# Kernel optimization log

Hardware: AMD Instinct MI355X
Metric: run time of the kernel (lower is better)

Reference implementation:

```python
import jax, jax.numpy as jnp
import numpy as np

EMBED = 256
HEADS = 8
HEAD_DIM = EMBED // HEADS  # 32, even for RoPE
INIT_VAL = 1.0
HEADS_RANGE = 3.0


def rotate_every_two(x):
    # (x1, x2) -> (-x2, x1) on interleaved pairs of last dim
    x1 = x[..., ::2]
    x2 = x[..., 1::2]
    return jnp.stack([-x2, x1], axis=-1).reshape(x.shape)


def theta_shift(x, sin, cos):
    # x: [B, heads, H, W, D]; sin/cos: [H, W, D] broadcast over B, heads
    return x * cos + rotate_every_two(x) * sin


def rel_pos_2d(H, W):
    # RetNetRelPos2d: RoPE angles + per-head exponential decay mask
    angle = 1.0 / (10000.0 ** jnp.linspace(0.0, 1.0, HEAD_DIM // 2))
    angle = jnp.repeat(angle, 2)  # [D]
    idx = jnp.arange(H * W, dtype=jnp.float32)
    sin = jnp.sin(idx[:, None] * angle[None, :]).reshape(H, W, HEAD_DIM)
    cos = jnp.cos(idx[:, None] * angle[None, :]).reshape(H, W, HEAD_DIM)
    h_idx = jnp.arange(HEADS, dtype=jnp.float32)
    decay = jnp.log(1.0 - 2.0 ** (-INIT_VAL - HEADS_RANGE * h_idx / HEADS))  # [heads]
    gh, gw = jnp.meshgrid(jnp.arange(H), jnp.arange(W), indexing='ij')
    grid = jnp.stack([gh, gw], axis=-1).reshape(H * W, 2)  # [N,2]
    dist = jnp.abs(grid[:, None, :] - grid[None, :, :]).sum(-1)  # [N,N] L1 distance
    mask = dist[None, :, :].astype(jnp.float32) * decay[:, None, None]  # [heads,N,N]
    return sin, cos, mask


def setup_inputs() -> dict:
    key = jax.random.key(0)
    ks = jax.random.split(key, 8)
    B, H, W, C = 2, 48, 48, EMBED
    s = 0.02
    return {
        'x': jax.random.normal(ks[0], (B, H, W, C), jnp.float32),
        'Wq': jax.random.normal(ks[1], (C, C), jnp.float32) * s,
        'bq': jnp.zeros((C,), jnp.float32),
        'Wk': jax.random.normal(ks[2], (C, C), jnp.float32) * s,
        'bk': jnp.zeros((C,), jnp.float32),
        'Wv': jax.random.normal(ks[3], (C, C), jnp.float32) * s,
        'bv': jnp.zeros((C,), jnp.float32),
        'lepe_w': jax.random.normal(ks[4], (C, 1, 5, 5), jnp.float32) * s,  # depthwise 5x5
        'lepe_b': jnp.zeros((C,), jnp.float32),
        'Wo': jax.random.normal(ks[5], (C, C), jnp.float32) * s,
        'bo': jnp.zeros((C,), jnp.float32),
    }


def reference(x, Wq, bq, Wk, bk, Wv, bv, lepe_w, lepe_b, Wo, bo):
    B, H, W, C = x.shape
    N = H * W
    sin, cos, mask = rel_pos_2d(H, W)
    scaling = HEAD_DIM ** -0.5

    q = x @ Wq + bq
    k = (x @ Wk + bk) * scaling
    v = x @ Wv + bv

    # lepe: depthwise 5x5 conv on v (BHWC)
    lepe = jax.lax.conv_general_dilated(
        v.transpose(0, 3, 1, 2), lepe_w, (1, 1), 'SAME',
        feature_group_count=C, dimension_numbers=('NCHW', 'OIHW', 'NCHW'))
    lepe = lepe.transpose(0, 2, 3, 1) + lepe_b  # [B,H,W,C]

    def split_heads(t):
        return t.reshape(B, H, W, HEADS, HEAD_DIM).transpose(0, 3, 1, 2, 4)

    qr = theta_shift(split_heads(q), sin, cos).reshape(B, HEADS, N, HEAD_DIM)
    kr = theta_shift(split_heads(k), sin, cos).reshape(B, HEADS, N, HEAD_DIM)
    vv = split_heads(v).reshape(B, HEADS, N, HEAD_DIM)

    attn = jnp.einsum('bhnd,bhmd->bhnm', qr, kr) + mask[None]  # [B,heads,N,N]
    attn = jax.nn.softmax(attn, axis=-1)
    out = jnp.einsum('bhnm,bhmd->bhnd', attn, vv)
    out = out.transpose(0, 2, 1, 3).reshape(B, H, W, C)
    out = out + lepe
    return out @ Wo + bo
```

## Files before the change

### kernel.cpp

```cpp
#include <hip/hip_runtime.h>
#include <hip/hip_bf16.h>
#include <math.h>

#define NN 2304
#define ROWSZ 4608
#define SZ (ROWSZ*256)

typedef __attribute__((ext_vector_type(8))) short short8;
typedef __attribute__((ext_vector_type(4))) float f32x4;

__device__ __forceinline__ float bf2f(unsigned short u) {
    return __uint_as_float(((unsigned int)u) << 16);
}
__device__ __forceinline__ unsigned short f2bf(float f) {
    unsigned int u = __float_as_uint(f);
    u += 0x7FFFu + ((u >> 16) & 1u);
    return (unsigned short)(u >> 16);
}
__device__ __forceinline__ unsigned int pack_bf2(float a, float b) {
    return (unsigned int)f2bf(a) | ((unsigned int)f2bf(b) << 16);
}

__device__ __forceinline__ float ub2f(unsigned int v, int r) {
#if defined(__has_builtin)
#if __has_builtin(__builtin_amdgcn_cvt_f32_ubyte0)
    switch (r) {
        case 0: return __builtin_amdgcn_cvt_f32_ubyte0(v);
        case 1: return __builtin_amdgcn_cvt_f32_ubyte1(v);
        case 2: return __builtin_amdgcn_cvt_f32_ubyte2(v);
        default: return __builtin_amdgcn_cvt_f32_ubyte3(v);
    }
#else
    return (float)((v >> (8*r)) & 0xFFu);
#endif
#else
    return (float)((v >> (8*r)) & 0xFFu);
#endif
}

template<int F32>
__device__ __forceinline__ float ldin(const void* p, int i) {
    if constexpr (F32) return ((const float*)p)[i];
    else return bf2f(((const unsigned short*)p)[i]);
}

__global__ void detect_kernel(const unsigned int* __restrict__ x, int* __restrict__ flag) {
    int t = threadIdx.x;
    int cnt = 0;
    for (int i = t; i < 256; i += 64) {
        unsigned int e = (x[i] >> 7) & 0xFFu;
        cnt += (e < 87u || e > 167u) ? 1 : 0;
    }
    #pragma unroll
    for (int o = 32; o; o >>= 1) cnt += __shfl_down(cnt, o);
    if (t == 0) *flag = (cnt >= 32) ? 1 : 0;
}

__global__ __launch_bounds__(256) void dist_kernel(unsigned char* __restrict__ D) {
    const int nq = blockIdx.x;
    const int yq = (nq*21846) >> 20, xq = nq - yq*48;
    unsigned int* drow = reinterpret_cast<unsigned int*>(D + (size_t)nq*NN);
    for (int idx = threadIdx.x; idx < 576; idx += 256) {
        const int kp0 = idx*4;
        unsigned int wv = 0;
        #pragma unroll
        for (int r = 0; r < 4; ++r) {
            int kp = kp0 + r;
            int yk = (kp*21846) >> 20;
            int xk = kp - yk*48;
            unsigned int dist = __usad((unsigned)yq, (unsigned)yk,
                                __usad((unsigned)xq, (unsigned)xk, 0u));
            wv |= dist << (8*r);
        }
        drow[idx] = wv;
    }
}

template<int F32>
__device__ __forceinline__ void qkv_body(
    const void* __restrict__ x,
    const void* __restrict__ Wq, const void* __restrict__ bq,
    const void* __restrict__ Wk, const void* __restrict__ bk,
    const void* __restrict__ Wv, const void* __restrict__ bv,
    unsigned short* __restrict__ q, unsigned short* __restrict__ k,
    unsigned short* __restrict__ v, unsigned short* __restrict__ vT,
    float* __restrict__ xs)
{
    const int t = threadIdx.x;
    const int by = blockIdx.y;
    const int row0 = blockIdx.x * 16;
    #pragma unroll
    for (int pass = 0; pass < 2; ++pass) {
        int e = pass*2048 + t*8;
        if constexpr (F32) {
            const float* xp = (const float*)x + row0*256 + e;
            float4 a0 = *reinterpret_cast<const float4*>(xp);
            float4 a1 = *reinterpret_cast<const float4*>(xp + 4);
            *reinterpret_cast<float4*>(&xs[e])   = a0;
            *reinterpret_cast<float4*>(&xs[e+4]) = a1;
        } else {
            const unsigned short* xp = (const unsigned short*)x + row0*256 + e;
            uint4 raw = *reinterpret_cast<const uint4*>(xp);
            const unsigned short* us = reinterpret_cast<const unsigned short*>(&raw);
            #pragma unroll
            for (int j = 0; j < 8; ++j) xs[e + j] = bf2f(us[j]);
        }
    }
    __syncthreads();
    const void* Wsel = (by == 0) ? Wq : (by == 1) ? Wk : Wv;
    const void* bsel = (by == 0) ? bq : (by == 1) ? bk : bv;
    float a[16];
    const float bv0 = ldin<F32>(bsel, t);
    #pragma unroll
    for (int r = 0; r < 16; ++r) a[r] = bv0;
    for (int i0 = 0; i0 < 256; i0 += 4) {
        float w0 = ldin<F32>(Wsel, (i0+0)*256 + t);
        float w1 = ldin<F32>(Wsel, (i0+1)*256 + t);
        float w2 = ldin<F32>(Wsel, (i0+2)*256 + t);
        float w3 = ldin<F32>(Wsel, (i0+3)*256 + t);
        #pragma unroll
        for (int r = 0; r < 16; ++r) {
            float4 xv = *reinterpret_cast<const float4*>(&xs[r*256 + i0]);
            a[r] = fmaf(xv.w,w3, fmaf(xv.z,w2, fmaf(xv.y,w1, fmaf(xv.x,w0, a[r]))));
        }
    }
    if (by == 2) {
        const int b = (row0 >= NN) ? 1 : 0;
        const int n0 = row0 - b*NN;
        const int h = t >> 5, d = t & 31;
        unsigned int vp[8];
        #pragma unroll
        for (int r = 0; r < 16; ++r) v[(row0 + r)*256 + t] = f2bf(a[r]);
        #pragma unroll
        for (int r = 0; r < 8; ++r) vp[r] = pack_bf2(a[2*r], a[2*r+1]);
        unsigned short* vt = vT + ((size_t)(b*8 + h)*32 + d)*NN + n0;
        *reinterpret_cast<uint4*>(vt)     = make_uint4(vp[0], vp[1], vp[2], vp[3]);
        *reinterpret_cast<uint4*>(vt + 8) = make_uint4(vp[4], vp[5], vp[6], vp[7]);
    } else {
        const float scaling = 0.17677669529663687f;
        const float log2e   = 1.4426950408889634f;
        const int j = (t & 31) >> 1;
        const float ang = exp2f((float)j * (-0.8858474919699633f));
        const bool odd = t & 1;
        unsigned short* dst = (by == 0) ? q : k;
        const float mul = (by == 0) ? 1.0f : scaling * log2e;
        #pragma unroll
        for (int r = 0; r < 16; ++r) {
            int bn = row0 + r;
            int n = bn >= NN ? bn - NN : bn;
            float sv, cv;
            sincosf((float)n * ang, &sv, &cv);
            float ap = __shfl_xor(a[r], 1);
            float val = odd ? fmaf(a[r], cv, ap*sv) : fmaf(a[r], cv, -ap*sv);
            dst[bn*256 + t] = f2bf(val * mul);
        }
    }
}

__global__ __launch_bounds__(256) void qkv_kernel(
    const void* __restrict__ x,
    const void* __restrict__ Wq, const void* __restrict__ bq,
    const void* __restrict__ Wk, const void* __restrict__ bk,
    const void* __restrict__ Wv, const void* __restrict__ bv,
    const int* __restrict__ flag,
    unsigned short* __restrict__ q, unsigned short* __restrict__ k,
    unsigned short* __restrict__ v, unsigned short* __restrict__ vT)
{
    __shared__ float xs[16*256];
    if (*flag) qkv_body<1>(x, Wq, bq, Wk, bk, Wv, bv, q, k, v, vT, xs);
    else       qkv_body<0>(x, Wq, bq, Wk, bk, Wv, bv, q, k, v, vT, xs);
}

template<int F32>
__device__ __forceinline__ void lepe_body(const unsigned short* __restrict__ v,
    const void* __restrict__ w, const void* __restrict__ wb,
    unsigned short* __restrict__ lepe)
{
    int c = threadIdx.x;
    int pos = blockIdx.x;
    int b  = pos >= NN ? 1 : 0;
    int yx = pos - b*NN;
    int y  = (yx*21846) >> 20;
    int xx = yx - y*48;
    float acc = ldin<F32>(wb, c);
    #pragma unroll
    for (int ky = 0; ky < 5; ++ky) {
        int yy = y + ky - 2;
        if ((unsigned)yy >= 48u) continue;
        #pragma unroll
        for (int kx = 0; kx < 5; ++kx) {
            int xc = xx + kx - 2;
            if ((unsigned)xc >= 48u) continue;
            acc = fmaf(bf2f(v[((b*NN + yy*48 + xc)<<8) + c]), ldin<F32>(w, c*25 + ky*5 + kx), acc);
        }
    }
    lepe[(pos<<8) + c] = f2bf(acc);
}

__global__ __launch_bounds__(256) void lepe_kernel(const unsigned short* __restrict__ v,
    const void* __restrict__ w, const void* __restrict__ wb,
    const int* __restrict__ flag, unsigned short* __restrict__ lepe)
{
    if (*flag) lepe_body<1>(v, w, wb, lepe);
    else       lepe_body<0>(v, w, wb, lepe);
}

template<int DIRECT>
__global__ __launch_bounds__(256) void attn_kernel(
    const unsigned short* __restrict__ q, const unsigned short* __restrict__ k,
    const unsigned short* __restrict__ vT, const unsigned char* __restrict__ D,
    unsigned short* __restrict__ o, float* __restrict__ pacc, float* __restrict__ pl)
{
    __shared__ char smem[27648];
    const int t = threadIdx.x;
    const int w = t >> 6, lane = t & 63;
    const int q16 = lane & 15, quad = lane >> 4;
    char* PsB = smem + 19456 + w*2048;
    const int bh = blockIdx.y, b = bh >> 3, h = bh & 7;
    const int q0 = blockIdx.x*64 + w*16;
    const int nq = q0 + q16;
    const float decay2 = log2f(1.0f - exp2f(-1.0f - 0.375f*(float)h));
    short8 qfrag = *reinterpret_cast<const short8*>(q + ((size_t)(b*NN + nq))*256 + h*32 + quad*8);
    f32x4 acc0 = {0.f,0.f,0.f,0.f}, acc1 = {0.f,0.f,0.f,0.f};
    const f32x4 zero = {0.f,0.f,0.f,0.f};
    float lacc = 0.0f;
    const unsigned short* kbase = k + (size_t)(b*NN)*256 + h*32;
    const unsigned short* vtb = vT + (size_t)bh*32*NN;
    const unsigned char* Dbase = D + (size_t)nq*NN + quad*4;
    const int skr = t >> 2, skp = t & 3;
    const int svd = t >> 3, svp = t & 7;
    const int psW = q16*16 + (quad & 1)*8;
    const int qsh = quad >> 1;
    const int nchunk = 36 / gridDim.z;
    const int kt0 = blockIdx.z * nchunk;

    {
        uint4 kraw = *reinterpret_cast<const uint4*>(kbase + (kt0*64 + skr)*256 + skp*8);
        uint4 vraw = *reinterpret_cast<const uint4*>(vtb + svd*NN + kt0*64 + svp*8);
        *reinterpret_cast<uint4*>(smem + skr*80 + skp*16) = kraw;
        *reinterpret_cast<uint4*>(smem + 5120 + svd*144 + svp*16) = vraw;
    }
    __syncthreads();

    int cur = 0;
    for (int kc = 0; kc < nchunk; ++kc) {
        const int kt = kt0 + kc;
        const int ktn = (kc + 1 < nchunk) ? kt + 1 : kt;
        uint4 nk = *reinterpret_cast<const uint4*>(kbase + (ktn*64 + skr)*256 + skp*8);
        uint4 nv = *reinterpret_cast<const uint4*>(vtb + svd*NN + ktn*64 + svp*8);
        unsigned int dw[4];
        #pragma unroll
        for (int tt = 0; tt < 4; ++tt)
            dw[tt] = *reinterpret_cast<const unsigned int*>(Dbase + kt*64 + tt*16);
        char* KsB = smem + cur*9728;
        char* VtB = KsB + 5120;
        f32x4 st[4];
        #pragma unroll
        for (int tt = 0; tt < 4; ++tt) {
            short8 kf = *reinterpret_cast<const short8*>(KsB + (tt*16 + q16)*80 + quad*16);
            st[tt] = __builtin_amdgcn_mfma_f32_16x16x32_bf16(kf, qfrag, zero, 0, 0, 0);
        }
        unsigned int pk[8];
        float lsum = 0.0f;
        #pragma unroll
        for (int tt = 0; tt < 4; ++tt) {
            float p[4];
            #pragma unroll
            for (int r = 0; r < 4; ++r) {
                p[r] = exp2f(fmaf(decay2, ub2f(dw[tt], r), st[tt][r]));
                lsum += p[r];
            }
            pk[tt*2]   = __builtin_amdgcn_perm(__float_as_uint(p[1]), __float_as_uint(p[0]), 0x07060302);
            pk[tt*2+1] = __builtin_amdgcn_perm(__float_as_uint(p[3]), __float_as_uint(p[2]), 0x07060302);
        }
        lacc += lsum;
        #pragma unroll
        for (int tt = 0; tt < 4; ++tt) {
            uint2 pp; pp.x = pk[tt*2]; pp.y = pk[tt*2+1];
            *reinterpret_cast<uint2*>(PsB + (tt >> 1)*1024 + (((tt*2) + qsh) & 3)*256 + psW) = pp;
        }
        #pragma unroll
        for (int kh = 0; kh < 2; ++kh) {
            short8 pf = *reinterpret_cast<const short8*>(PsB + kh*1024 + lane*16);
            short8 v0 = *reinterpret_cast<const short8*>(VtB + q16*144 + kh*64 + quad*16);
            short8 v1 = *reinterpret_cast<const short8*>(VtB + (16 + q16)*144 + kh*64 + quad*16);
            acc0 = __builtin_amdgcn_mfma_f32_16x16x32_bf16(v0, pf, acc0, 0, 0, 0);
            acc1 = __builtin_amdgcn_mfma_f32_16x16x32_bf16(v1, pf, acc1, 0, 0, 0);
        }
        char* KsN = smem + (cur^1)*9728;
        *reinterpret_cast<uint4*>(KsN + skr*80 + skp*16) = nk;
        *reinterpret_cast<uint4*>(KsN + 5120 + svd*144 + svp*16) = nv;
        __syncthreads();
        cur ^= 1;
    }
    lacc += __shfl_xor(lacc, 16);
    lacc += __shfl_xor(lacc, 32);
    if constexpr (DIRECT) {
        float invl = 1.0f / lacc;
        unsigned short* orow = o + ((size_t)(b*NN + nq))*256 + h*32;
        uint2 w0, w1;
        w0.x = pack_bf2(acc0[0]*invl, acc0[1]*invl);
        w0.y = pack_bf2(acc0[2]*invl, acc0[3]*invl);
        w1.x = pack_bf2(acc1[0]*invl, acc1[1]*invl);
        w1.y = pack_bf2(acc1[2]*invl, acc1[3]*invl);
        *reinterpret_cast<uint2*>(orow + quad*4)      = w0;
        *reinterpret_cast<uint2*>(orow + 16 + quad*4) = w1;
    } else {
        float* pb = pacc + ((size_t)(blockIdx.z*16 + bh)*NN + nq)*32;
        *reinterpret_cast<f32x4*>(pb + quad*4)      = acc0;
        *reinterpret_cast<f32x4*>(pb + 16 + quad*4) = acc1;
        if (quad == 0) pl[((size_t)blockIdx.z*16 + bh)*NN + nq] = lacc;
    }
}

template<int F32>
__device__ __forceinline__ void out_body(
    const unsigned short* __restrict__ o,
    const float* __restrict__ pacc, const float* __restrict__ pl,
    const unsigned short* __restrict__ lp,
    const void* __restrict__ Wo, const void* __restrict__ bo,
    void* __restrict__ out, float* __restrict__ as, int nsplit)
{
    const int t = threadIdx.x;
    const int row0 = blockIdx.x * 8;
    {
        const int e = t*8;
        const int r = t >> 5;
        const int nqr = row0 + r;
        const int ch = e & 255;
        uint4 ub = *reinterpret_cast<const uint4*>(lp + nqr*256 + ch);
        const unsigned short* bu = reinterpret_cast<const unsigned short*>(&ub);
        if (nsplit == 0) {
            uint4 ua = *reinterpret_cast<const uint4*>(o + nqr*256 + ch);
            const unsigned short* au = reinterpret_cast<const unsigned short*>(&ua);
            #pragma unroll
            for (int jj = 0; jj < 8; ++jj) as[e+jj] = bf2f(au[jj]) + bf2f(bu[jj]);
        } else {
            const int b = nqr >= NN ? 1 : 0;
            const int nq = nqr - b*NN;
            const int h = ch >> 5, d = ch & 31;
            const int bh = b*8 + h;
            float s[8] = {0.f,0.f,0.f,0.f,0.f,0.f,0.f,0.f};
            float lsum = 0.0f;
            for (int p = 0; p < nsplit; ++p) {
                const float* pb = pacc + ((size_t)(p*16 + bh)*NN + nq)*32 + d;
                f32x4 v0 = *reinterpret_cast<const f32x4*>(pb);
                f32x4 v1 = *reinterpret_cast<const f32x4*>(pb + 4);
                #pragma unroll
                for (int jj = 0; jj < 4; ++jj) { s[jj] += v0[jj]; s[4+jj] += v1[jj]; }
                lsum += pl[((size_t)p*16 + bh)*NN + nq];
            }
            float invl = 1.0f / lsum;
            #pragma unroll
            for (int jj = 0; jj < 8; ++jj) as[e+jj] = fmaf(s[jj], invl, bf2f(bu[jj]));
        }
    }
    __syncthreads();
    float a[8];
    const float bv = ldin<F32>(bo, t);
    #pragma unroll
    for (int r = 0; r < 8; ++r) a[r] = bv;
    for (int i0 = 0; i0 < 256; i0 += 4) {
        float w0 = ldin<F32>(Wo, (i0+0)*256 + t);
        float w1 = ldin<F32>(Wo, (i0+1)*256 + t);
        float w2 = ldin<F32>(Wo, (i0+2)*256 + t);
        float w3 = ldin<F32>(Wo, (i0+3)*256 + t);
        #pragma unroll
        for (int r = 0; r < 8; ++r) {
            float4 xv = *reinterpret_cast<const float4*>(&as[r*256 + i0]);
            a[r] = fmaf(xv.w,w3, fmaf(xv.z,w2, fmaf(xv.y,w1, fmaf(xv.x,w0, a[r]))));
        }
    }
    #pragma unroll
    for (int r = 0; r < 8; ++r) {
        int idx = (row0+r)*256 + t;
        if constexpr (F32) ((float*)out)[idx] = a[r];
        else ((unsigned short*)out)[idx] = f2bf(a[r]);
    }
}

__global__ __launch_bounds__(256) void out_kernel(
    const unsigned short* __restrict__ o,
    const float* __restrict__ pacc, const float* __restrict__ pl,
    const unsigned short* __restrict__ lp,
    const void* __restrict__ Wo, const void* __restrict__ bo,
    const int* __restrict__ flag, void* __restrict__ out, int nsplit)
{
    __shared__ float as[8*256];
    if (*flag) out_body<1>(o, pacc, pl, lp, Wo, bo, out, as, nsplit);
    else       out_body<0>(o, pacc, pl, lp, Wo, bo, out, as, nsplit);
}

extern "C" void kernel_launch(void* const* d_in, const int* in_sizes, int n_in,
                              void* d_out, int out_size, void* d_ws, size_t ws_size,
                              hipStream_t stream)
{
    const void* x  = d_in[0];
    const void* Wq = d_in[1];
    const void* bq = d_in[2];
    const void* Wk = d_in[3];
    const void* bk = d_in[4];
    const void* Wv = d_in[5];
    const void* bv = d_in[6];
    const void* lw = d_in[7];
    const void* lb = d_in[8];
    const void* Wo = d_in[9];
    const void* bo = d_in[10];

    int* flag = (int*)d_ws;
    unsigned short* qb   = (unsigned short*)((char*)d_ws + 256);
    unsigned short* kbuf = qb   + (size_t)SZ;
    unsigned short* vbuf = kbuf + (size_t)SZ;
    unsigned short* obuf = vbuf + (size_t)SZ;
    unsigned short* lbuf = obuf + (size_t)SZ;
    unsigned short* vtb  = lbuf + (size_t)SZ;
    unsigned char*  Dtab = (unsigned char*)(vtb + (size_t)SZ);

    const size_t base = 256 + 6*(size_t)SZ*2 + (size_t)NN*NN;
    const size_t per_split = (size_t)16*NN*32*4 + (size_t)16*NN*4;
    int nsplit = 0;
    if      (ws_size >= base + 4*per_split) nsplit = 4;
    else if (ws_size >= base + 2*per_split) nsplit = 2;
    else if (ws_size >= base + 1*per_split) nsplit = 1;
    float* pacc = (float*)((char*)d_ws + base);
    float* pl   = pacc + (size_t)(nsplit ? nsplit : 1)*16*NN*32;

    detect_kernel<<<1, 64, 0, stream>>>((const unsigned int*)x, flag);
    dist_kernel<<<NN, 256, 0, stream>>>(Dtab);
    qkv_kernel<<<dim3(288,3), 256, 0, stream>>>(x, Wq, bq, Wk, bk, Wv, bv, flag, qb, kbuf, vbuf, vtb);
    lepe_kernel<<<4608, 256, 0, stream>>>(vbuf, lw, lb, flag, lbuf);
    if (nsplit) {
        attn_kernel<0><<<dim3(36, 16, nsplit), 256, 0, stream>>>(qb, kbuf, vtb, Dtab, obuf, pacc, pl);
    } else {
        attn_kernel<1><<<dim3(36, 16, 1), 256, 0, stream>>>(qb, kbuf, vtb, Dtab, obuf, pacc, pl);
    }
    out_kernel<<<576, 256, 0, stream>>>(obuf, pacc, pl, lbuf, Wo, bo, flag, d_out, nsplit);
}
```

Before: 235.5 us.

## Replace scalar FP32 QKV projection with bf16 MFMA kernel plus prep passes

Replaces the scalar-FMA QKV projection with an MFMA bf16 GEMM kernel. Two new prep kernels convert x to bf16 and transpose, scale and convert the weights and biases. The RoPE sin/cos table is now computed once in dist_kernel instead of per element. The projection core moves onto matrix cores with a double-buffered LDS weight pipeline and staged coalesced output writes, at the cost of extra launches, more workspace, and bf16 rounding of x and the weights.

```diff
diff --git a/kernel.cpp b/kernel.cpp
--- a/kernel.cpp
+++ b/kernel.cpp
@@ -56,7 +56,8 @@
     if (t == 0) *flag = (cnt >= 32) ? 1 : 0;
 }
 
-__global__ __launch_bounds__(256) void dist_kernel(unsigned char* __restrict__ D) {
+__global__ __launch_bounds__(256) void dist_kernel(unsigned char* __restrict__ D,
+                                                   float2* __restrict__ scT) {
     const int nq = blockIdx.x;
     const int yq = (nq*21846) >> 20, xq = nq - yq*48;
     unsigned int* drow = reinterpret_cast<unsigned int*>(D + (size_t)nq*NN);
@@ -74,101 +75,185 @@
         }
         drow[idx] = wv;
     }
-}
-
-template<int F32>
-__device__ __forceinline__ void qkv_body(
-    const void* __restrict__ x,
-    const void* __restrict__ Wq, const void* __restrict__ bq,
-    const void* __restrict__ Wk, const void* __restrict__ bk,
-    const void* __restrict__ Wv, const void* __restrict__ bv,
-    unsigned short* __restrict__ q, unsigned short* __restrict__ k,
-    unsigned short* __restrict__ v, unsigned short* __restrict__ vT,
-    float* __restrict__ xs)
-{
-    const int t = threadIdx.x;
-    const int by = blockIdx.y;
-    const int row0 = blockIdx.x * 16;
-    #pragma unroll
-    for (int pass = 0; pass < 2; ++pass) {
-        int e = pass*2048 + t*8;
-        if constexpr (F32) {
-            const float* xp = (const float*)x + row0*256 + e;
-            float4 a0 = *reinterpret_cast<const float4*>(xp);
-            float4 a1 = *reinterpret_cast<const float4*>(xp + 4);
-            *reinterpret_cast<float4*>(&xs[e])   = a0;
-            *reinterpret_cast<float4*>(&xs[e+4]) = a1;
-        } else {
-            const unsigned short* xp = (const unsigned short*)x + row0*256 + e;
-            uint4 raw = *reinterpret_cast<const uint4*>(xp);
-            const unsigned short* us = reinterpret_cast<const unsigned short*>(&raw);
-            #pragma unroll
-            for (int j = 0; j < 8; ++j) xs[e + j] = bf2f(us[j]);
-        }
-    }
-    __syncthreads();
-    const void* Wsel = (by == 0) ? Wq : (by == 1) ? Wk : Wv;
-    const void* bsel = (by == 0) ? bq : (by == 1) ? bk : bv;
-    float a[16];
-    const float bv0 = ldin<F32>(bsel, t);
-    #pragma unroll
-    for (int r = 0; r < 16; ++r) a[r] = bv0;
-    for (int i0 = 0; i0 < 256; i0 += 4) {
-        float w0 = ldin<F32>(Wsel, (i0+0)*256 + t);
-        float w1 = ldin<F32>(Wsel, (i0+1)*256 + t);
-        float w2 = ldin<F32>(Wsel, (i0+2)*256 + t);
-        float w3 = ldin<F32>(Wsel, (i0+3)*256 + t);
-        #pragma unroll
-        for (int r = 0; r < 16; ++r) {
-            float4 xv = *reinterpret_cast<const float4*>(&xs[r*256 + i0]);
-            a[r] = fmaf(xv.w,w3, fmaf(xv.z,w2, fmaf(xv.y,w1, fmaf(xv.x,w0, a[r]))));
-        }
-    }
-    if (by == 2) {
-        const int b = (row0 >= NN) ? 1 : 0;
-        const int n0 = row0 - b*NN;
-        const int h = t >> 5, d = t & 31;
-        unsigned int vp[8];
-        #pragma unroll
-        for (int r = 0; r < 16; ++r) v[(row0 + r)*256 + t] = f2bf(a[r]);
-        #pragma unroll
-        for (int r = 0; r < 8; ++r) vp[r] = pack_bf2(a[2*r], a[2*r+1]);
-        unsigned short* vt = vT + ((size_t)(b*8 + h)*32 + d)*NN + n0;
-        *reinterpret_cast<uint4*>(vt)     = make_uint4(vp[0], vp[1], vp[2], vp[3]);
-        *reinterpret_cast<uint4*>(vt + 8) = make_uint4(vp[4], vp[5], vp[6], vp[7]);
+    if (threadIdx.x < 16) {
+        const int j = threadIdx.x;
+        const float ang = exp2f((float)j * (-0.8858474919699633f));
+        float sv, cv;
+        sincosf((float)nq * ang, &sv, &cv);
+        scT[nq*16 + j] = make_float2(sv, cv);
+    }
+}
+
+__global__ __launch_bounds__(256) void xprep_kernel(const void* __restrict__ x,
+    const int* __restrict__ flag, unsigned short* __restrict__ xb)
+{
+    const int e = (blockIdx.x*256 + threadIdx.x) * 8;
+    if (*flag) {
+        const float* xp = (const float*)x + e;
+        float4 a0 = *reinterpret_cast<const float4*>(xp);
+        float4 a1 = *reinterpret_cast<const float4*>(xp + 4);
+        uint4 o;
+        o.x = pack_bf2(a0.x, a0.y); o.y = pack_bf2(a0.z, a0.w);
+        o.z = pack_bf2(a1.x, a1.y); o.w = pack_bf2(a1.z, a1.w);
+        *reinterpret_cast<uint4*>(xb + e) = o;
     } else {
-        const float scaling = 0.17677669529663687f;
-        const float log2e   = 1.4426950408889634f;
-        const int j = (t & 31) >> 1;
-        const float ang = exp2f((float)j * (-0.8858474919699633f));
-        const bool odd = t & 1;
-        unsigned short* dst = (by == 0) ? q : k;
-        const float mul = (by == 0) ? 1.0f : scaling * log2e;
-        #pragma unroll
-        for (int r = 0; r < 16; ++r) {
-            int bn = row0 + r;
-            int n = bn >= NN ? bn - NN : bn;
-            float sv, cv;
-            sincosf((float)n * ang, &sv, &cv);
-            float ap = __shfl_xor(a[r], 1);
-            float val = odd ? fmaf(a[r], cv, ap*sv) : fmaf(a[r], cv, -ap*sv);
-            dst[bn*256 + t] = f2bf(val * mul);
-        }
-    }
-}
-
-__global__ __launch_bounds__(256) void qkv_kernel(
-    const void* __restrict__ x,
+        *reinterpret_cast<uint4*>(xb + e) =
+            *reinterpret_cast<const uint4*>((const unsigned short*)x + e);
+    }
+}
+
+__global__ __launch_bounds__(256) void wprep_kernel(
     const void* __restrict__ Wq, const void* __restrict__ bq,
     const void* __restrict__ Wk, const void* __restrict__ bk,
     const void* __restrict__ Wv, const void* __restrict__ bv,
     const int* __restrict__ flag,
+    unsigned short* __restrict__ Wt, float* __restrict__ bb)
+{
+    __shared__ float wsh[256][17];
+    const int t = threadIdx.x;
+    const int m = blockIdx.y;
+    const int oc0 = blockIdx.x * 16;
+    const void* W  = (m == 0) ? Wq : (m == 1) ? Wk : Wv;
+    const void* bs = (m == 0) ? bq : (m == 1) ? bk : bv;
+    const float scale = (m == 1) ? 0.17677669529663687f * 1.4426950408889634f : 1.0f;
+    const int F = *flag;
+    #pragma unroll
+    for (int j2 = 0; j2 < 16; ++j2)
+        wsh[t][j2] = F ? ((const float*)W)[t*256 + oc0 + j2]
+                       : bf2f(((const unsigned short*)W)[t*256 + oc0 + j2]);
+    __syncthreads();
+    const int j = t >> 4, seg = t & 15;
+    unsigned int u[8];
+    #pragma unroll
+    for (int i = 0; i < 8; ++i) {
+        float v0 = wsh[seg*16 + 2*i][j]     * scale;
+        float v1 = wsh[seg*16 + 2*i + 1][j] * scale;
+        u[i] = pack_bf2(v0, v1);
+    }
+    unsigned short* drow = Wt + ((size_t)(m*256 + oc0 + j))*256 + seg*16;
+    *reinterpret_cast<uint4*>(drow)     = make_uint4(u[0], u[1], u[2], u[3]);
+    *reinterpret_cast<uint4*>(drow + 8) = make_uint4(u[4], u[5], u[6], u[7]);
+    if (blockIdx.x == 0)
+        bb[m*256 + t] = (F ? ((const float*)bs)[t]
+                           : bf2f(((const unsigned short*)bs)[t])) * scale;
+}
+
+__global__ __launch_bounds__(256) void qkv_mfma(
+    const unsigned short* __restrict__ xb, const unsigned short* __restrict__ Wt,
+    const float* __restrict__ bb, const float2* __restrict__ scT,
     unsigned short* __restrict__ q, unsigned short* __restrict__ k,
     unsigned short* __restrict__ v, unsigned short* __restrict__ vT)
 {
-    __shared__ float xs[16*256];
-    if (*flag) qkv_body<1>(x, Wq, bq, Wk, bk, Wv, bv, q, k, v, vT, xs);
-    else       qkv_body<0>(x, Wq, bq, Wk, bk, Wv, bv, q, k, v, vT, xs);
+    __shared__ __align__(16) char smem[43136];
+    char* sc_lds = smem + 40960;
+    const int t = threadIdx.x;
+    const int w = t >> 6, lane = t & 63;
+    const int q16 = lane & 15, quad = lane >> 4;
+    const int m = blockIdx.y;
+    const int tok0 = blockIdx.x * 16;
+    const int b = (tok0 >= NN) ? 1 : 0;
+    const int n0 = tok0 - b*NN;
+
+    {
+        float2 sv = scT[(size_t)(n0 + (t >> 4))*16 + (t & 15)];
+        *reinterpret_cast<float2*>(sc_lds + (t >> 4)*136 + (t & 15)*8) = sv;
+    }
+    short8 af[8];
+    #pragma unroll
+    for (int kk = 0; kk < 8; ++kk)
+        af[kk] = *reinterpret_cast<const short8*>(
+            xb + (size_t)(tok0 + q16)*256 + kk*32 + quad*8);
+
+    const unsigned short* Wm = Wt + (size_t)m*256*256;
+    {
+        const unsigned short* src = Wm + (size_t)t*256;
+        #pragma unroll
+        for (int s = 0; s < 4; ++s)
+            *reinterpret_cast<uint4*>(smem + t*80 + s*16) =
+                *reinterpret_cast<const uint4*>(src + s*8);
+    }
+    __syncthreads();
+
+    f32x4 acc[4];
+    #pragma unroll
+    for (int tt = 0; tt < 4; ++tt) acc[tt] = (f32x4){0.f, 0.f, 0.f, 0.f};
+    int cur = 0;
+    for (int kk = 0; kk < 8; ++kk) {
+        const int kkn = (kk < 7) ? kk + 1 : 7;
+        uint4 nw[4];
+        const unsigned short* src = Wm + (size_t)t*256 + kkn*32;
+        #pragma unroll
+        for (int s = 0; s < 4; ++s) nw[s] = *reinterpret_cast<const uint4*>(src + s*8);
+        char* Wl = smem + cur*20480;
+        #pragma unroll
+        for (int tt = 0; tt < 4; ++tt) {
+            short8 bf = *reinterpret_cast<const short8*>(
+                Wl + (w*64 + tt*16 + q16)*80 + quad*16);
+            acc[tt] = __builtin_amdgcn_mfma_f32_16x16x32_bf16(af[kk], bf, acc[tt], 0, 0, 0);
+        }
+        char* Wn = smem + (cur ^ 1)*20480;
+        #pragma unroll
+        for (int s = 0; s < 4; ++s)
+            *reinterpret_cast<uint4*>(Wn + t*80 + s*16) = nw[s];
+        __syncthreads();
+        cur ^= 1;
+    }
+
+    char* ostage = smem;
+    float bias[4];
+    #pragma unroll
+    for (int tt = 0; tt < 4; ++tt) bias[tt] = bb[m*256 + w*64 + tt*16 + q16];
+    if (m < 2) {
+        const int odd = q16 & 1;
+        #pragma unroll
+        for (int tt = 0; tt < 4; ++tt) {
+            const int j = ((tt & 1) << 3) + (q16 >> 1);
+            #pragma unroll
+            for (int r = 0; r < 4; ++r) {
+                const int tokL = quad*4 + r;
+                float a = acc[tt][r] + bias[tt];
+                float ap = __shfl_xor(a, 1);
+                float2 sc = *reinterpret_cast<const float2*>(sc_lds + tokL*136 + j*8);
+                float val = odd ? fmaf(a, sc.y, ap*sc.x) : fmaf(a, sc.y, -ap*sc.x);
+                *reinterpret_cast<unsigned short*>(
+                    ostage + tokL*528 + (w*64 + tt*16 + q16)*2) = f2bf(val);
+            }
+        }
+    } else {
+        #pragma unroll
+        for (int tt = 0; tt < 4; ++tt) {
+            #pragma unroll
+            for (int r = 0; r < 4; ++r)
+                *reinterpret_cast<unsigned short*>(
+                    ostage + (quad*4 + r)*528 + (w*64 + tt*16 + q16)*2)
+                    = f2bf(acc[tt][r] + bias[tt]);
+        }
+    }
+    __syncthreads();
+    unsigned short* dst = (m == 0) ? q : (m == 1) ? k : v;
+    {
+        char* p = ostage + (t >> 4)*528 + (t & 15)*32;
+        uint4 a0 = *reinterpret_cast<uint4*>(p);
+        uint4 a1 = *reinterpret_cast<uint4*>(p + 16);
+        unsigned short* drow = dst + (size_t)(tok0 + (t >> 4))*256 + (t & 15)*16;
+        *reinterpret_cast<uint4*>(drow)     = a0;
+        *reinterpret_cast<uint4*>(drow + 8) = a1;
+    }
+    if (m == 2) {
+        const int h = t >> 5, d = t & 31;
+        unsigned int vp[8];
+        #pragma unroll
+        for (int i = 0; i < 8; ++i) {
+            unsigned short e0 = *reinterpret_cast<unsigned short*>(
+                ostage + (2*i)*528 + (h*32 + d)*2);
+            unsigned short e1 = *reinterpret_cast<unsigned short*>(
+                ostage + (2*i + 1)*528 + (h*32 + d)*2);
+            vp[i] = (unsigned int)e0 | ((unsigned int)e1 << 16);
+        }
+        unsigned short* vt = vT + ((size_t)(b*8 + h)*32 + d)*NN + n0;
+        *reinterpret_cast<uint4*>(vt)     = make_uint4(vp[0], vp[1], vp[2], vp[3]);
+        *reinterpret_cast<uint4*>(vt + 8) = make_uint4(vp[4], vp[5], vp[6], vp[7]);
+    }
 }
 
 template<int F32>
@@ -415,8 +500,14 @@
     unsigned short* lbuf = obuf + (size_t)SZ;
     unsigned short* vtb  = lbuf + (size_t)SZ;
     unsigned char*  Dtab = (unsigned char*)(vtb + (size_t)SZ);
-
-    const size_t base = 256 + 6*(size_t)SZ*2 + (size_t)NN*NN;
+    float2* scT = (float2*)(Dtab + (size_t)NN*NN);
+    unsigned short* xb = (unsigned short*)(scT + (size_t)NN*16);
+    unsigned short* Wt = xb + (size_t)SZ;
+    float* bb = (float*)(Wt + (size_t)3*256*256);
+
+    const size_t base = 256 + 6*(size_t)SZ*2 + (size_t)NN*NN
+                      + (size_t)NN*16*8 + (size_t)SZ*2
+                      + (size_t)3*256*256*2 + (size_t)3*256*4;
     const size_t per_split = (size_t)16*NN*32*4 + (size_t)16*NN*4;
     int nsplit = 0;
     if      (ws_size >= base + 4*per_split) nsplit = 4;
@@ -426,8 +517,10 @@
     float* pl   = pacc + (size_t)(nsplit ? nsplit : 1)*16*NN*32;
 
     detect_kernel<<<1, 64, 0, stream>>>((const unsigned int*)x, flag);
-    dist_kernel<<<NN, 256, 0, stream>>>(Dtab);
-    qkv_kernel<<<dim3(288,3), 256, 0, stream>>>(x, Wq, bq, Wk, bk, Wv, bv, flag, qb, kbuf, vbuf, vtb);
+    dist_kernel<<<NN, 256, 0, stream>>>(Dtab, scT);
+    xprep_kernel<<<576, 256, 0, stream>>>(x, flag, xb);
+    wprep_kernel<<<dim3(16,3), 256, 0, stream>>>(Wq, bq, Wk, bk, Wv, bv, flag, Wt, bb);
+    qkv_mfma<<<dim3(288,3), 256, 0, stream>>>(xb, Wt, bb, scT, qb, kbuf, vbuf, vtb);
     lepe_kernel<<<4608, 256, 0, stream>>>(vbuf, lw, lb, flag, lbuf);
     if (nsplit) {
         attn_kernel<0><<<dim3(36, 16, nsplit), 256, 0, stream>>>(qb, kbuf, vtb, Dtab, obuf, pacc, pl);
```

After: 220.8 us. -6.2%, faster.
